# Optimization experiments

Hardware: AMD Instinct MI355X
Metric: run time of the kernel (lower is better)

## Reference

```python
import jax, jax.numpy as jnp
import numpy as np

D_MODEL = 1024
D_HEAD = 64
B, S = 4, 2048


def setup_inputs() -> dict:
    key = jax.random.key(0)
    k1, k2, k3, k4 = jax.random.split(key, 4)
    residual_stream = jax.random.normal(k1, (B, S, D_MODEL), dtype=jnp.float32)
    # torch.nn.Linear weights are [out_features, in_features]
    Wq = jax.random.normal(k2, (D_HEAD, D_MODEL), dtype=jnp.float32) * 0.02
    Wk = jax.random.normal(k3, (D_HEAD, D_MODEL), dtype=jnp.float32) * 0.02
    Wv = jax.random.normal(k4, (D_HEAD, D_MODEL), dtype=jnp.float32) * 0.02
    return {"residual_stream": residual_stream, "Wq": Wq, "Wk": Wk, "Wv": Wv}


def reference(residual_stream, Wq, Wk, Wv):
    # Linear projections (no bias): y = x @ W.T
    q = jnp.einsum('bsd,hd->bsh', residual_stream, Wq)  # [B,S,d_head]
    k = jnp.einsum('bsd,hd->bsh', residual_stream, Wk)
    v = jnp.einsum('bsd,hd->bsh', residual_stream, Wv)
    # NOTE: module scales by 1/sqrt(d_model), not 1/sqrt(d_head)
    scale = 1.0 / jnp.sqrt(jnp.float32(D_MODEL))
    scores = jnp.einsum('bqh,bkh->bqk', q, k) * scale  # [B,S,S]
    # causal mask: lower-triangular allowed
    s = residual_stream.shape[1]
    causal = jnp.tril(jnp.ones((s, s), dtype=bool))
    scores = jnp.where(causal[None, :, :], scores, -jnp.inf)
    attn = jax.nn.softmax(scores, axis=-1)
    # dropout_chance=0.0 (eval/deterministic) -> identity
    return jnp.einsum('bqk,bkh->bqh', attn, v)  # [B,S,d_head]
```

## Files before the change

### kernel.cpp

```cpp
#include <hip/hip_runtime.h>
#include <hip/hip_bf16.h>

#define NB 4
#define SEQ 2048
#define DM 1024
#define DH 64

typedef __attribute__((ext_vector_type(8))) short bf16x8;
typedef __attribute__((ext_vector_type(4))) float f32x4;
typedef __attribute__((ext_vector_type(4))) short short4v;

__device__ inline short f2bf(float f) {
  union { float f; unsigned u; } x; x.f = f;
  unsigned r = x.u + 0x7FFFu + ((x.u >> 16) & 1u);
  return (short)(r >> 16);
}

__global__ __launch_bounds__(256) void wconv_kernel(
    const float* __restrict__ Wq, const float* __restrict__ Wk,
    const float* __restrict__ Wv, short* __restrict__ wbf)
{
  const int tid = blockIdx.x * 256 + threadIdx.x;
  const int base = tid * 8;
  const int row = base >> 10;
  const int col = base & 1023;
  const float* src = (row < 64) ? Wq : (row < 128) ? Wk : Wv;
  src += (size_t)(row & 63) * DM + col;
  f32x4 f0 = ((const f32x4*)src)[0];
  f32x4 f1 = ((const f32x4*)src)[1];
  bf16x8 h = { f2bf(f0[0]), f2bf(f0[1]), f2bf(f0[2]), f2bf(f0[3]),
               f2bf(f1[0]), f2bf(f1[1]), f2bf(f1[2]), f2bf(f1[3]) };
  *(bf16x8*)(wbf + (size_t)row * DM + col) = h;
}

__global__ __launch_bounds__(512) void proj_kernel(
    const float* __restrict__ X, const short* __restrict__ wbf,
    short* __restrict__ qout, short* __restrict__ kout,
    short* __restrict__ vtout)
{
  __shared__ short x_lds[2][32][80];
  __shared__ short w_lds[2][192][80];

  const int t = threadIdx.x;
  const int l = t & 63;
  const int w = t >> 6;
  const int m0 = blockIdx.x * 32;

  f32x4 acc[3];
#pragma unroll
  for (int i = 0; i < 3; i++) acc[i] = (f32x4){0.f, 0.f, 0.f, 0.f};

  const int xr = t >> 4;
  const int xc = (t & 15) * 4;
  const int wr = t >> 3;
  const int wc = (t & 7) * 8;

  {
    f32x4 f = *(const f32x4*)(X + (size_t)(m0 + xr) * DM + xc);
    short4v h = { f2bf(f[0]), f2bf(f[1]), f2bf(f[2]), f2bf(f[3]) };
    *(short4v*)&x_lds[0][xr][xc] = h;
#pragma unroll
    for (int s = 0; s < 3; s++)
      *(bf16x8*)&w_lds[0][s * 64 + wr][wc] =
          *(const bf16x8*)(wbf + (size_t)(s * 64 + wr) * DM + wc);
  }
  __syncthreads();

  for (int it = 0; it < 16; it++) {
    const int buf = it & 1;
    const bool pf = (it < 15);

    f32x4 xf;
    bf16x8 wf0, wf1, wf2;
    if (pf) {
      const int k1 = (it + 1) * 64;
      xf  = *(const f32x4*)(X + (size_t)(m0 + xr) * DM + k1 + xc);
      wf0 = *(const bf16x8*)(wbf + (size_t)(0 * 64 + wr) * DM + k1 + wc);
      wf1 = *(const bf16x8*)(wbf + (size_t)(1 * 64 + wr) * DM + k1 + wc);
      wf2 = *(const bf16x8*)(wbf + (size_t)(2 * 64 + wr) * DM + k1 + wc);
    }

    const short* xp = &x_lds[buf][(w & 1) * 16 + (l & 15)][(l >> 4) << 3];
    bf16x8 a0 = *(const bf16x8*)xp;
    bf16x8 a1 = *(const bf16x8*)(xp + 32);
#pragma unroll
    for (int nf = 0; nf < 3; nf++) {
      const int cf = (w >> 1) * 3 + nf;
      const short* wp = &w_lds[buf][cf * 16 + (l & 15)][(l >> 4) << 3];
      bf16x8 b0 = *(const bf16x8*)wp;
      bf16x8 b1 = *(const bf16x8*)(wp + 32);
      acc[nf] = __builtin_amdgcn_mfma_f32_16x16x32_bf16(a0, b0, acc[nf], 0, 0, 0);
      acc[nf] = __builtin_amdgcn_mfma_f32_16x16x32_bf16(a1, b1, acc[nf], 0, 0, 0);
    }

    if (pf) {
      short4v h = { f2bf(xf[0]), f2bf(xf[1]), f2bf(xf[2]), f2bf(xf[3]) };
      *(short4v*)&x_lds[buf ^ 1][xr][xc] = h;
      *(bf16x8*)&w_lds[buf ^ 1][0 * 64 + wr][wc] = wf0;
      *(bf16x8*)&w_lds[buf ^ 1][1 * 64 + wr][wc] = wf1;
      *(bf16x8*)&w_lds[buf ^ 1][2 * 64 + wr][wc] = wf2;
    }
    __syncthreads();
  }

  const int rowb = m0 + (w & 1) * 16 + ((l >> 4) << 2);
#pragma unroll
  for (int nf = 0; nf < 3; nf++) {
    const int c = ((w >> 1) * 3 + nf) * 16 + (l & 15);
#pragma unroll
    for (int j = 0; j < 4; j++) {
      const int row = rowb + j;
      const float v = acc[nf][j];
      if (c < 64) {
        qout[row * DH + c] = f2bf(v * 0.03125f);
      } else if (c < 128) {
        kout[row * DH + (c - 64)] = f2bf(v);
      } else {
        const int b = row >> 11, s = row & (SEQ - 1);
        vtout[b * (DH * SEQ) + (c - 128) * SEQ + s] = f2bf(v);
      }
    }
  }
}

__global__ __launch_bounds__(256) void flash_kernel(
    const short* __restrict__ qin, const short* __restrict__ kin,
    const short* __restrict__ vtin, float* __restrict__ po,
    float* __restrict__ pm, float* __restrict__ pl,
    const int nck, const int cht)
{
  __shared__ short k_lds[2][64][72];
  __shared__ short vt_lds[2][64][72];
  __shared__ short p_lds[4][16][72];

  const int qt = blockIdx.x;
  const int ck = blockIdx.y;
  const int t0 = ck * cht;
  if (t0 > qt) return;
  const int b = blockIdx.z;

  const int t = threadIdx.x;
  const int l = t & 63;
  const int w = t >> 6;
  const int q0 = qt * 64;
  const int tend = min(t0 + cht, qt + 1);

  const short* qb = qin  + (size_t)b * SEQ * DH;
  const short* kb = kin  + (size_t)b * SEQ * DH;
  const short* vb = vtin + (size_t)b * DH * SEQ;

  const short* qr = qb + (size_t)(q0 + w * 16 + (l & 15)) * DH + ((l >> 4) << 3);
  const bf16x8 qf0 = *(const bf16x8*)qr;
  const bf16x8 qf1 = *(const bf16x8*)(qr + 32);

  f32x4 o[4];
#pragma unroll
  for (int i = 0; i < 4; i++) o[i] = (f32x4){0.f, 0.f, 0.f, 0.f};
  float m_run[4] = {-1e30f, -1e30f, -1e30f, -1e30f};
  float l_run[4] = {0.f, 0.f, 0.f, 0.f};

  const int sr = t >> 3;
  const int sc = (t & 7) * 8;

  {
    const int j0 = t0 * 64;
#pragma unroll
    for (int i = 0; i < 2; i++) {
      const int r = sr + i * 32;
      *(bf16x8*)&k_lds[0][r][sc]  = *(const bf16x8*)(kb + (size_t)(j0 + r) * DH + sc);
      *(bf16x8*)&vt_lds[0][r][sc] = *(const bf16x8*)(vb + (size_t)r * SEQ + j0 + sc);
    }
  }
  __syncthreads();

  for (int tt = t0; tt < tend; tt++) {
    const int bi = (tt - t0) & 1;
    const int j0 = tt * 64;
    const bool pf = (tt + 1 < tend);

    bf16x8 kpf0, kpf1, vpf0, vpf1;
    if (pf) {
      const int j1 = j0 + 64;
      kpf0 = *(const bf16x8*)(kb + (size_t)(j1 + sr) * DH + sc);
      kpf1 = *(const bf16x8*)(kb + (size_t)(j1 + sr + 32) * DH + sc);
      vpf0 = *(const bf16x8*)(vb + (size_t)sr * SEQ + j1 + sc);
      vpf1 = *(const bf16x8*)(vb + (size_t)(sr + 32) * SEQ + j1 + sc);
    }

    f32x4 s[4];
#pragma unroll
    for (int nf = 0; nf < 4; nf++) {
      const short* kr = &k_lds[bi][nf * 16 + (l & 15)][(l >> 4) << 3];
      bf16x8 b0 = *(const bf16x8*)kr;
      bf16x8 b1 = *(const bf16x8*)(kr + 32);
      f32x4 a = (f32x4){0.f, 0.f, 0.f, 0.f};
      a = __builtin_amdgcn_mfma_f32_16x16x32_bf16(qf0, b0, a, 0, 0, 0);
      a = __builtin_amdgcn_mfma_f32_16x16x32_bf16(qf1, b1, a, 0, 0, 0);
      s[nf] = a;
    }

    {
      const int growb = q0 + w * 16 + ((l >> 4) << 2);
#pragma unroll
      for (int nf = 0; nf < 4; nf++) {
        const int gcol = j0 + nf * 16 + (l & 15);
#pragma unroll
        for (int j = 0; j < 4; j++)
          if (gcol > growb + j) s[nf][j] = -1e30f;
      }
    }

    float alpha[4];
#pragma unroll
    for (int j = 0; j < 4; j++) {
      float tm = fmaxf(fmaxf(s[0][j], s[1][j]), fmaxf(s[2][j], s[3][j]));
      tm = fmaxf(tm, __shfl_xor(tm, 1));
      tm = fmaxf(tm, __shfl_xor(tm, 2));
      tm = fmaxf(tm, __shfl_xor(tm, 4));
      tm = fmaxf(tm, __shfl_xor(tm, 8));
      const float mn = fmaxf(m_run[j], tm);
      alpha[j] = exp2f((m_run[j] - mn) * 1.44269504f);
      m_run[j] = mn;
      float rs = 0.f;
#pragma unroll
      for (int nf = 0; nf < 4; nf++) {
        const float p = exp2f((s[nf][j] - mn) * 1.44269504f);
        s[nf][j] = p;
        rs += p;
      }
      rs += __shfl_xor(rs, 1);
      rs += __shfl_xor(rs, 2);
      rs += __shfl_xor(rs, 4);
      rs += __shfl_xor(rs, 8);
      l_run[j] = l_run[j] * alpha[j] + rs;
    }
#pragma unroll
    for (int df = 0; df < 4; df++)
#pragma unroll
      for (int j = 0; j < 4; j++) o[df][j] *= alpha[j];

#pragma unroll
    for (int nf = 0; nf < 4; nf++)
#pragma unroll
      for (int j = 0; j < 4; j++)
        p_lds[w][((l >> 4) << 2) + j][nf * 16 + (l & 15)] = f2bf(s[nf][j]);

    asm volatile("s_waitcnt lgkmcnt(0)" ::: "memory");
    __builtin_amdgcn_sched_barrier(0);

#pragma unroll
    for (int ks = 0; ks < 2; ks++) {
      const short* pr = &p_lds[w][l & 15][ks * 32 + ((l >> 4) << 3)];
      const bf16x8 pa = *(const bf16x8*)pr;
#pragma unroll
      for (int df = 0; df < 4; df++) {
        const short* vr = &vt_lds[bi][df * 16 + (l & 15)][ks * 32 + ((l >> 4) << 3)];
        const bf16x8 vf = *(const bf16x8*)vr;
        o[df] = __builtin_amdgcn_mfma_f32_16x16x32_bf16(pa, vf, o[df], 0, 0, 0);
      }
    }

    if (pf) {
      *(bf16x8*)&k_lds[bi ^ 1][sr][sc]       = kpf0;
      *(bf16x8*)&k_lds[bi ^ 1][sr + 32][sc]  = kpf1;
      *(bf16x8*)&vt_lds[bi ^ 1][sr][sc]      = vpf0;
      *(bf16x8*)&vt_lds[bi ^ 1][sr + 32][sc] = vpf1;
    }
    __syncthreads();
  }

  const int rowb = q0 + w * 16 + ((l >> 4) << 2);
#pragma unroll
  for (int j = 0; j < 4; j++) {
    const size_t rowg = (size_t)b * SEQ + rowb + j;
#pragma unroll
    for (int df = 0; df < 4; df++)
      po[(rowg * nck + ck) * DH + df * 16 + (l & 15)] = o[df][j];
    if ((l & 15) == 0) {
      pm[rowg * nck + ck] = m_run[j];
      pl[rowg * nck + ck] = l_run[j];
    }
  }
}

__global__ __launch_bounds__(256) void merge_kernel(
    const float* __restrict__ po, const float* __restrict__ pm,
    const float* __restrict__ pl, float* __restrict__ out,
    const int nck, const int ckshift)
{
  const int gid = blockIdx.x * 256 + threadIdx.x;
  const int r = gid >> 6;
  const int d = gid & 63;
  const int s = r & (SEQ - 1);
  const int C = (s >> ckshift) + 1;

  float m = -1e30f;
  for (int c = 0; c < C; c++) m = fmaxf(m, pm[r * nck + c]);
  float den = 0.f, num = 0.f;
  for (int c = 0; c < C; c++) {
    const float wgt = exp2f((pm[r * nck + c] - m) * 1.44269504f);
    den += pl[r * nck + c] * wgt;
    num += po[(size_t)(r * nck + c) * DH + d] * wgt;
  }
  out[gid] = num / den;
}

extern "C" void kernel_launch(void* const* d_in, const int* in_sizes, int n_in,
                              void* d_out, int out_size, void* d_ws, size_t ws_size,
                              hipStream_t stream) {
  const float* X  = (const float*)d_in[0];
  const float* Wq = (const float*)d_in[1];
  const float* Wk = (const float*)d_in[2];
  const float* Wv = (const float*)d_in[3];

  const size_t nrow = (size_t)NB * SEQ;
  short* qws  = (short*)d_ws;
  short* kws  = qws + nrow * DH;
  short* vtws = kws + nrow * DH;
  float* po   = (float*)(vtws + nrow * DH);
  short* wbf  = (short*)po;
  const size_t qkv_bytes = 3 * nrow * DH * sizeof(short);

  int nck, cht, ckshift;
  {
    const size_t need4 = qkv_bytes + nrow * 4 * (DH + 2) * sizeof(float);
    if (ws_size >= need4) { nck = 4; cht = 8;  ckshift = 9;  }
    else                  { nck = 1; cht = 32; ckshift = 11; }
  }
  float* pm = po + nrow * nck * DH;
  float* pl = pm + nrow * nck;

  wconv_kernel<<<dim3(96), 256, 0, stream>>>(Wq, Wk, Wv, wbf);
  proj_kernel<<<dim3(NB * SEQ / 32), 512, 0, stream>>>(X, wbf, qws, kws, vtws);
  flash_kernel<<<dim3(SEQ / 64, nck, NB), 256, 0, stream>>>(qws, kws, vtws, po, pm, pl, nck, cht);
  merge_kernel<<<dim3(NB * SEQ * DH / 256), 256, 0, stream>>>(po, pm, pl, (float*)d_out, nck, ckshift);
}
```

Baseline: 52.88 us.

## Split projection over output halves with direct-to-LDS weight loads and XOR swizzle

After: 54.96 us. 3.9% more time.

```diff
diff --git a/kernel.cpp b/kernel.cpp
--- a/kernel.cpp
+++ b/kernel.cpp
@@ -14,6 +14,12 @@
   union { float f; unsigned u; } x; x.f = f;
   unsigned r = x.u + 0x7FFFu + ((x.u >> 16) & 1u);
   return (short)(r >> 16);
+}
+
+__device__ inline void gload_lds16(const short* g, short* l) {
+  __builtin_amdgcn_global_load_lds(
+      (const __attribute__((address_space(1))) void*)g,
+      (__attribute__((address_space(3))) void*)l, 16, 0, 0);
 }
 
 __global__ __launch_bounds__(256) void wconv_kernel(
@@ -30,87 +36,102 @@
   f32x4 f1 = ((const f32x4*)src)[1];
   bf16x8 h = { f2bf(f0[0]), f2bf(f0[1]), f2bf(f0[2]), f2bf(f0[3]),
                f2bf(f1[0]), f2bf(f1[1]), f2bf(f1[2]), f2bf(f1[3]) };
-  *(bf16x8*)(wbf + (size_t)row * DM + col) = h;
-}
-
-__global__ __launch_bounds__(512) void proj_kernel(
+  const int c16 = col >> 3;
+  const int c16s = (c16 & ~7) | ((c16 ^ row) & 7);
+  *(bf16x8*)(wbf + (size_t)row * DM + c16s * 8) = h;
+}
+
+__global__ __launch_bounds__(256) void proj_kernel(
     const float* __restrict__ X, const short* __restrict__ wbf,
     short* __restrict__ qout, short* __restrict__ kout,
     short* __restrict__ vtout)
 {
-  __shared__ short x_lds[2][32][80];
-  __shared__ short w_lds[2][192][80];
+  __shared__ short w_lds[2][96 * 64];
+  __shared__ short x_lds[2][32 * 64];
 
   const int t = threadIdx.x;
   const int l = t & 63;
   const int w = t >> 6;
   const int m0 = blockIdx.x * 32;
+  const int h  = blockIdx.y;
+
+  const int mw = w & 1;
+  const int ng = w >> 1;
 
   f32x4 acc[3];
 #pragma unroll
   for (int i = 0; i < 3; i++) acc[i] = (f32x4){0.f, 0.f, 0.f, 0.f};
 
-  const int xr = t >> 4;
-  const int xc = (t & 15) * 4;
-  const int wr = t >> 3;
-  const int wc = (t & 7) * 8;
-
+  const int xrow = t >> 3;
+  const int xch  = t & 7;
+  const float* xsrc = X + (size_t)(m0 + xrow) * DM + xch * 8;
+  const int xdst = xrow * 64 + ((xch ^ (xrow & 7)) << 3);
+
+  const short* wsrc_base = wbf + (size_t)h * 96 * DM;
+
+#pragma unroll
+  for (int i = 0; i < 3; i++) {
+    const int c = (w * 3 + i) * 64 + l;
+    const short* g = wsrc_base + (size_t)(c >> 3) * DM + (c & 7) * 8;
+    gload_lds16(g, &w_lds[0][(w * 3 + i) * 512]);
+  }
   {
-    f32x4 f = *(const f32x4*)(X + (size_t)(m0 + xr) * DM + xc);
-    short4v h = { f2bf(f[0]), f2bf(f[1]), f2bf(f[2]), f2bf(f[3]) };
-    *(short4v*)&x_lds[0][xr][xc] = h;
-#pragma unroll
-    for (int s = 0; s < 3; s++)
-      *(bf16x8*)&w_lds[0][s * 64 + wr][wc] =
-          *(const bf16x8*)(wbf + (size_t)(s * 64 + wr) * DM + wc);
+    f32x4 f0 = ((const f32x4*)xsrc)[0];
+    f32x4 f1 = ((const f32x4*)xsrc)[1];
+    bf16x8 hx = { f2bf(f0[0]), f2bf(f0[1]), f2bf(f0[2]), f2bf(f0[3]),
+                  f2bf(f1[0]), f2bf(f1[1]), f2bf(f1[2]), f2bf(f1[3]) };
+    *(bf16x8*)&x_lds[0][xdst] = hx;
   }
   __syncthreads();
 
   for (int it = 0; it < 16; it++) {
     const int buf = it & 1;
     const bool pf = (it < 15);
-
-    f32x4 xf;
-    bf16x8 wf0, wf1, wf2;
+    const int k1 = (it + 1) * 64;
+
+    f32x4 f0, f1;
     if (pf) {
-      const int k1 = (it + 1) * 64;
-      xf  = *(const f32x4*)(X + (size_t)(m0 + xr) * DM + k1 + xc);
-      wf0 = *(const bf16x8*)(wbf + (size_t)(0 * 64 + wr) * DM + k1 + wc);
-      wf1 = *(const bf16x8*)(wbf + (size_t)(1 * 64 + wr) * DM + k1 + wc);
-      wf2 = *(const bf16x8*)(wbf + (size_t)(2 * 64 + wr) * DM + k1 + wc);
-    }
-
-    const short* xp = &x_lds[buf][(w & 1) * 16 + (l & 15)][(l >> 4) << 3];
-    bf16x8 a0 = *(const bf16x8*)xp;
-    bf16x8 a1 = *(const bf16x8*)(xp + 32);
-#pragma unroll
-    for (int nf = 0; nf < 3; nf++) {
-      const int cf = (w >> 1) * 3 + nf;
-      const short* wp = &w_lds[buf][cf * 16 + (l & 15)][(l >> 4) << 3];
-      bf16x8 b0 = *(const bf16x8*)wp;
-      bf16x8 b1 = *(const bf16x8*)(wp + 32);
-      acc[nf] = __builtin_amdgcn_mfma_f32_16x16x32_bf16(a0, b0, acc[nf], 0, 0, 0);
-      acc[nf] = __builtin_amdgcn_mfma_f32_16x16x32_bf16(a1, b1, acc[nf], 0, 0, 0);
+#pragma unroll
+      for (int i = 0; i < 3; i++) {
+        const int c = (w * 3 + i) * 64 + l;
+        const short* g = wsrc_base + (size_t)(c >> 3) * DM + k1 + (c & 7) * 8;
+        gload_lds16(g, &w_lds[buf ^ 1][(w * 3 + i) * 512]);
+      }
+      f0 = ((const f32x4*)(xsrc + k1))[0];
+      f1 = ((const f32x4*)(xsrc + k1))[1];
+    }
+
+    {
+      const int arow = mw * 16 + (l & 15);
+      const int ac = l >> 4;
+      bf16x8 a0 = *(const bf16x8*)&x_lds[buf][arow * 64 + ((ac ^ (arow & 7)) << 3)];
+      bf16x8 a1 = *(const bf16x8*)&x_lds[buf][arow * 64 + (((ac + 4) ^ (arow & 7)) << 3)];
+#pragma unroll
+      for (int j = 0; j < 3; j++) {
+        const int wrow = (ng * 3 + j) * 16 + (l & 15);
+        bf16x8 b0 = *(const bf16x8*)&w_lds[buf][wrow * 64 + ((ac ^ (wrow & 7)) << 3)];
+        bf16x8 b1 = *(const bf16x8*)&w_lds[buf][wrow * 64 + (((ac + 4) ^ (wrow & 7)) << 3)];
+        acc[j] = __builtin_amdgcn_mfma_f32_16x16x32_bf16(a0, b0, acc[j], 0, 0, 0);
+        acc[j] = __builtin_amdgcn_mfma_f32_16x16x32_bf16(a1, b1, acc[j], 0, 0, 0);
+      }
     }
 
     if (pf) {
-      short4v h = { f2bf(xf[0]), f2bf(xf[1]), f2bf(xf[2]), f2bf(xf[3]) };
-      *(short4v*)&x_lds[buf ^ 1][xr][xc] = h;
-      *(bf16x8*)&w_lds[buf ^ 1][0 * 64 + wr][wc] = wf0;
-      *(bf16x8*)&w_lds[buf ^ 1][1 * 64 + wr][wc] = wf1;
-      *(bf16x8*)&w_lds[buf ^ 1][2 * 64 + wr][wc] = wf2;
+      bf16x8 hx = { f2bf(f0[0]), f2bf(f0[1]), f2bf(f0[2]), f2bf(f0[3]),
+                    f2bf(f1[0]), f2bf(f1[1]), f2bf(f1[2]), f2bf(f1[3]) };
+      *(bf16x8*)&x_lds[buf ^ 1][xdst] = hx;
     }
     __syncthreads();
   }
 
-  const int rowb = m0 + (w & 1) * 16 + ((l >> 4) << 2);
-#pragma unroll
-  for (int nf = 0; nf < 3; nf++) {
-    const int c = ((w >> 1) * 3 + nf) * 16 + (l & 15);
-#pragma unroll
-    for (int j = 0; j < 4; j++) {
-      const int row = rowb + j;
-      const float v = acc[nf][j];
+  const int rowb = m0 + mw * 16 + ((l >> 4) << 2);
+#pragma unroll
+  for (int j = 0; j < 3; j++) {
+    const int c = h * 96 + (ng * 3 + j) * 16 + (l & 15);
+#pragma unroll
+    for (int jj = 0; jj < 4; jj++) {
+      const int row = rowb + jj;
+      const float v = acc[j][jj];
       if (c < 64) {
         qout[row * DH + c] = f2bf(v * 0.03125f);
       } else if (c < 128) {
@@ -317,8 +338,6 @@
   short* qws  = (short*)d_ws;
   short* kws  = qws + nrow * DH;
   short* vtws = kws + nrow * DH;
-  float* po   = (float*)(vtws + nrow * DH);
-  short* wbf  = (short*)po;
   const size_t qkv_bytes = 3 * nrow * DH * sizeof(short);
 
   int nck, cht, ckshift;
@@ -327,11 +346,13 @@
     if (ws_size >= need4) { nck = 4; cht = 8;  ckshift = 9;  }
     else                  { nck = 1; cht = 32; ckshift = 11; }
   }
-  float* pm = po + nrow * nck * DH;
-  float* pl = pm + nrow * nck;
+  float* po  = (float*)(vtws + nrow * DH);
+  short* wbf = (short*)po;
+  float* pm  = po + nrow * nck * DH;
+  float* pl  = pm + nrow * nck;
 
   wconv_kernel<<<dim3(96), 256, 0, stream>>>(Wq, Wk, Wv, wbf);
-  proj_kernel<<<dim3(NB * SEQ / 32), 512, 0, stream>>>(X, wbf, qws, kws, vtws);
+  proj_kernel<<<dim3(256, 2), 256, 0, stream>>>(X, wbf, qws, kws, vtws);
   flash_kernel<<<dim3(SEQ / 64, nck, NB), 256, 0, stream>>>(qws, kws, vtws, po, pm, pl, nck, cht);
   merge_kernel<<<dim3(NB * SEQ * DH / 256), 256, 0, stream>>>(po, pm, pl, (float*)d_out, nck, ckshift);
 }
```
